# Performance work log

Measured on AMD Instinct MI355X. Metric: run time of the kernel, lower is better.

## Reference

```python
import jax, jax.numpy as jnp
import numpy as np

N, E, G = 50000, 400000, 500
F_IN, D_H, D_EMB = 92, 256, 128
EPS = 1e-5

def _ln(x, g, b):
    # per-node LayerNorm over feature dim
    mu = jnp.mean(x, axis=-1, keepdims=True)
    var = jnp.mean(jnp.square(x - mu), axis=-1, keepdims=True)
    return (x - mu) * jax.lax.rsqrt(var + EPS) * g + b

def _gcn_conv(x, src, dst, W, b):
    # PyG GCNConv: add self-loops, symmetric normalization
    xw = x @ W                                    # [N, D_out]
    loop = jnp.arange(N, dtype=src.dtype)
    s = jnp.concatenate([src, loop])              # [E+N]
    d = jnp.concatenate([dst, loop])
    deg = jax.ops.segment_sum(jnp.ones_like(d, dtype=xw.dtype), d, num_segments=N)
    dinv = jnp.where(deg > 0, jax.lax.rsqrt(jnp.maximum(deg, 1.0)) * (deg > 0), 0.0)
    norm = dinv[s] * dinv[d]                      # [E+N]
    msg = xw[s] * norm[:, None]                   # gather + scale
    out = jax.ops.segment_sum(msg, d, num_segments=N)  # scatter-add
    return out + b

def setup_inputs() -> dict:
    key = jax.random.key(0)
    ks = jax.random.split(key, 12)
    def lin(k, fan_in, fan_out):
        bound = 1.0 / np.sqrt(fan_in)
        kw, kb = jax.random.split(k)
        W = jax.random.uniform(kw, (fan_in, fan_out), jnp.float32, -bound, bound)
        b = jax.random.uniform(kb, (fan_out,), jnp.float32, -bound, bound)
        return W, b
    x = jax.random.normal(ks[0], (N, F_IN), jnp.float32)
    edge_index = jax.random.randint(ks[1], (2, E), 0, N, jnp.int32)
    batch = jnp.sort(jax.random.randint(ks[2], (N,), 0, G, jnp.int32))
    nfc_W, nfc_b = lin(ks[3], F_IN, D_H)
    gc1_W, gc1_b = lin(ks[4], D_H, D_H)
    gc2_W, gc2_b = lin(ks[5], D_H, D_EMB)
    fc1_W, fc1_b = lin(ks[6], D_EMB, 64)
    fc2_W, fc2_b = lin(ks[7], 64, 1)
    return {
        "x": x, "edge_index": edge_index, "batch": batch,
        "nfc_W": nfc_W, "nfc_b": nfc_b,
        "gn1_g": jnp.ones((D_H,), jnp.float32), "gn1_b": jnp.zeros((D_H,), jnp.float32),
        "gc1_W": gc1_W, "gc1_b": gc1_b,
        "gn2_g": jnp.ones((D_EMB,), jnp.float32), "gn2_b": jnp.zeros((D_EMB,), jnp.float32),
        "gc2_W": gc2_W, "gc2_b": gc2_b,
        "fc1_W": fc1_W, "fc1_b": fc1_b,
        "fc2_W": fc2_W, "fc2_b": fc2_b,
    }

def reference(x, edge_index, batch, nfc_W, nfc_b, gn1_g, gn1_b, gc1_W, gc1_b,
              gn2_g, gn2_b, gc2_W, gc2_b, fc1_W, fc1_b, fc2_W, fc2_b):
    src, dst = edge_index[0], edge_index[1]
    lrelu = jax.nn.leaky_relu  # slope 0.01, matches F.leaky_relu default
    ha = lrelu(x @ nfc_W + nfc_b)
    ha = lrelu(_ln(_gcn_conv(ha, src, dst, gc1_W, gc1_b), gn1_g, gn1_b))
    ha = lrelu(_ln(_gcn_conv(ha, src, dst, gc2_W, gc2_b), gn2_g, gn2_b))
    # F.normalize(p=2, dim=1)
    ha = ha / jnp.maximum(jnp.linalg.norm(ha, axis=1, keepdims=True), 1e-12)
    hg = jax.ops.segment_sum(ha, batch, num_segments=G)   # global_add_pool
    h = lrelu(hg @ fc1_W + fc1_b)
    out = h @ fc2_W + fc2_b
    return out, ha
```

## Files before the change

kernel.cpp:

```cpp
#include <hip/hip_runtime.h>

#define NN 50000
#define EE 400000
#define GG 500
#define F_IN 92
#define KP1 96
#define D_H 256
#define D_EMB 128
#define PCH 16

typedef __attribute__((ext_vector_type(8))) short short8_t;
typedef __attribute__((ext_vector_type(4))) float floatx4;
typedef unsigned short u16;
typedef unsigned int u32;

__device__ __forceinline__ float lrelu(float v) { return v > 0.f ? v : 0.01f * v; }
__device__ __forceinline__ u16 f2b(float v) {
    union { float f; u32 u; } x; x.f = v;
    u32 r = x.u + 0x7FFFu + ((x.u >> 16) & 1u);
    return (u16)(r >> 16);
}
__device__ __forceinline__ float wave_allsum(float v) {
#pragma unroll
    for (int m = 1; m < 64; m <<= 1) v += __shfl_xor(v, m);
    return v;
}

__global__ void count_kernel(const int* __restrict__ dst, int* __restrict__ cnt, int E) {
    int e = blockIdx.x * blockDim.x + threadIdx.x;
    if (e < E) atomicAdd(&cnt[dst[e]], 1);
}

__global__ void scan1(const int* __restrict__ cnt, int* __restrict__ excl,
                      int* __restrict__ bsum, float* __restrict__ dinv, int n) {
    __shared__ int sm[256];
    int i = blockIdx.x * 256 + threadIdx.x;
    int v = (i < n) ? cnt[i] : 0;
    if (i < n) dinv[i] = rsqrtf((float)v + 1.0f);
    sm[threadIdx.x] = v;
    __syncthreads();
#pragma unroll
    for (int off = 1; off < 256; off <<= 1) {
        int t = (threadIdx.x >= off) ? sm[threadIdx.x - off] : 0;
        __syncthreads();
        sm[threadIdx.x] += t;
        __syncthreads();
    }
    if (i < n) excl[i] = sm[threadIdx.x] - v;
    if (threadIdx.x == 255) bsum[blockIdx.x] = sm[255];
}
__global__ void scan2(int* __restrict__ bsum, int nb) {
    __shared__ int sm[256];
    int v = (threadIdx.x < nb) ? bsum[threadIdx.x] : 0;
    sm[threadIdx.x] = v;
    __syncthreads();
#pragma unroll
    for (int off = 1; off < 256; off <<= 1) {
        int t = (threadIdx.x >= off) ? sm[threadIdx.x - off] : 0;
        __syncthreads();
        sm[threadIdx.x] += t;
        __syncthreads();
    }
    if (threadIdx.x < nb) bsum[threadIdx.x] = sm[threadIdx.x] - v;
}
__global__ void scan3(int* __restrict__ rowptr, const int* __restrict__ bsum, int n, int E) {
    int i = blockIdx.x * 256 + threadIdx.x;
    if (i < n) rowptr[i] += bsum[blockIdx.x];
    if (i == 0) rowptr[n] = E;
}
__global__ void scatter_kernel(const int* __restrict__ src, const int* __restrict__ dst,
                               const int* __restrict__ rowptr, int* __restrict__ cursor,
                               int* __restrict__ esrc, int E) {
    int e = blockIdx.x * blockDim.x + threadIdx.x;
    if (e >= E) return;
    int d = dst[e];
    int p = rowptr[d] + atomicAdd(&cursor[d], 1);
    esrc[p] = src[e];
}

__global__ void cast_pad_x(const float* __restrict__ x, u16* __restrict__ xb) {
    long i = (long)blockIdx.x * blockDim.x + threadIdx.x;
    if (i >= (long)NN * KP1) return;
    int row = (int)(i / KP1), col = (int)(i % KP1);
    float v = (col < F_IN) ? x[(long)row * F_IN + col] : 0.f;
    xb[i] = f2b(v);
}
__global__ void castT_W(const float* __restrict__ W, u16* __restrict__ Wt,
                        int K, int Nd, int Kp) {
    int i = blockIdx.x * blockDim.x + threadIdx.x;
    if (i >= Nd * Kp) return;
    int n = i / Kp, k = i % Kp;
    Wt[i] = f2b(k < K ? W[(long)k * Nd + n] : 0.f);
}

template <bool BIAS_ACT, bool ROW_SCALE>
__global__ __launch_bounds__(256) void gemm_mfma(const u16* __restrict__ A,
                                                 const u16* __restrict__ Wt,
                                                 const float* __restrict__ bias,
                                                 const float* __restrict__ rscale,
                                                 u16* __restrict__ out,
                                                 int M, int Ka, int Nd) {
    __shared__ u16 As[128][40];
    __shared__ u16 Bs[64][40];
    int tid = threadIdx.x;
    int wave = tid >> 6, lane = tid & 63;
    int lm = lane & 15, lk = lane >> 4;
    int m0 = blockIdx.x * 128, n0 = blockIdx.y * 64;
    int rowA = tid >> 1, skA = (tid & 1) * 16;
    int rowB = tid >> 2, skB = (tid & 3) * 8;
    int gmA = m0 + rowA;
    const u16* Ap = A + (size_t)gmA * Ka + skA;
    const u16* Bp = Wt + (size_t)(n0 + rowB) * Ka + skB;
    floatx4 acc[2][4] = {};
    for (int k0 = 0; k0 < Ka; k0 += 32) {
        uint4 a0 = make_uint4(0, 0, 0, 0), a1 = make_uint4(0, 0, 0, 0);
        if (gmA < M) {
            a0 = *(const uint4*)(Ap + k0);
            a1 = *(const uint4*)(Ap + k0 + 8);
        }
        uint4 bv = *(const uint4*)(Bp + k0);
        __syncthreads();
        *(uint4*)&As[rowA][skA] = a0;
        *(uint4*)&As[rowA][skA + 8] = a1;
        *(uint4*)&Bs[rowB][skB] = bv;
        __syncthreads();
        short8_t af0 = *(const short8_t*)&As[wave * 32 + lm][lk * 8];
        short8_t af1 = *(const short8_t*)&As[wave * 32 + 16 + lm][lk * 8];
#pragma unroll
        for (int c = 0; c < 4; ++c) {
            short8_t bf = *(const short8_t*)&Bs[c * 16 + lm][lk * 8];
            acc[0][c] = __builtin_amdgcn_mfma_f32_16x16x32_bf16(af0, bf, acc[0][c], 0, 0, 0);
            acc[1][c] = __builtin_amdgcn_mfma_f32_16x16x32_bf16(af1, bf, acc[1][c], 0, 0, 0);
        }
    }
#pragma unroll
    for (int h = 0; h < 2; ++h) {
#pragma unroll
        for (int r = 0; r < 4; ++r) {
            int gm = m0 + wave * 32 + h * 16 + lk * 4 + r;
            if (gm >= M) continue;
            float rs = ROW_SCALE ? rscale[gm] : 1.f;
#pragma unroll
            for (int c = 0; c < 4; ++c) {
                int gn = n0 + c * 16 + lm;
                float v = acc[h][c][r];
                if constexpr (BIAS_ACT) { v += bias[gn]; v = lrelu(v); }
                if constexpr (ROW_SCALE) v *= rs;
                out[(size_t)gm * Nd + gn] = f2b(v);
            }
        }
    }
}

template <int U>
__device__ __forceinline__ void loadrow(const u32* __restrict__ p, u32* r) {
    if constexpr (U == 2) { uint2 t = *(const uint2*)p; r[0] = t.x; r[1] = t.y; }
    else                  { r[0] = *p; }
}
template <int D, bool L2N, bool TOBF>
__global__ __launch_bounds__(256) void agg_ln(const u16* __restrict__ y,
                                              const int* __restrict__ rowptr,
                                              const int* __restrict__ esrc,
                                              const float* __restrict__ dinv,
                                              const float* __restrict__ bias,
                                              const float* __restrict__ gamma,
                                              const float* __restrict__ beta,
                                              u16* __restrict__ outb,
                                              float* __restrict__ outf) {
    constexpr int V = D / 64;
    constexpr int U = V / 2;
    constexpr int RW = D / 2;
    int wave = threadIdx.x >> 6, lane = threadIdx.x & 63;
    int i = blockIdx.x * 4 + wave;
    if (i >= NN) return;
    int beg = __builtin_amdgcn_readfirstlane(rowptr[i]);
    int end = __builtin_amdgcn_readfirstlane(rowptr[i + 1]);
    const u32* yu = (const u32*)y;
    const int lu = lane * U;
    float accL[U] = {}, accH[U] = {};
    u32 r[8][U];
    int k = beg;
    for (; k + 7 < end; k += 8) {
#pragma unroll
        for (int q = 0; q < 8; ++q) loadrow<U>(yu + (size_t)esrc[k + q] * RW + lu, r[q]);
#pragma unroll
        for (int j = 0; j < U; ++j) {
            float sL = 0.f, sH = 0.f;
#pragma unroll
            for (int q = 0; q < 8; ++q) {
                sL += __uint_as_float(r[q][j] << 16);
                sH += __uint_as_float(r[q][j] & 0xFFFF0000u);
            }
            accL[j] += sL; accH[j] += sH;
        }
    }
    for (; k + 3 < end; k += 4) {
#pragma unroll
        for (int q = 0; q < 4; ++q) loadrow<U>(yu + (size_t)esrc[k + q] * RW + lu, r[q]);
#pragma unroll
        for (int j = 0; j < U; ++j) {
            accL[j] += (__uint_as_float(r[0][j] << 16) + __uint_as_float(r[1][j] << 16))
                     + (__uint_as_float(r[2][j] << 16) + __uint_as_float(r[3][j] << 16));
            accH[j] += (__uint_as_float(r[0][j] & 0xFFFF0000u) + __uint_as_float(r[1][j] & 0xFFFF0000u))
                     + (__uint_as_float(r[2][j] & 0xFFFF0000u) + __uint_as_float(r[3][j] & 0xFFFF0000u));
        }
    }
    for (; k < end; ++k) {
        loadrow<U>(yu + (size_t)esrc[k] * RW + lu, r[0]);
#pragma unroll
        for (int j = 0; j < U; ++j) {
            accL[j] += __uint_as_float(r[0][j] << 16);
            accH[j] += __uint_as_float(r[0][j] & 0xFFFF0000u);
        }
    }
    loadrow<U>(yu + (size_t)i * RW + lu, r[0]);
#pragma unroll
    for (int j = 0; j < U; ++j) {
        accL[j] += __uint_as_float(r[0][j] << 16);
        accH[j] += __uint_as_float(r[0][j] & 0xFFFF0000u);
    }
    float di = dinv[i];
    float xv[V], lsum = 0.f;
#pragma unroll
    for (int j = 0; j < U; ++j) {
        xv[2 * j]     = accL[j] * di + bias[lane * V + 2 * j];
        xv[2 * j + 1] = accH[j] * di + bias[lane * V + 2 * j + 1];
    }
#pragma unroll
    for (int v = 0; v < V; ++v) lsum += xv[v];
    float mu = wave_allsum(lsum) * (1.0f / D);
    float l2 = 0.f;
#pragma unroll
    for (int v = 0; v < V; ++v) { xv[v] -= mu; l2 += xv[v] * xv[v]; }
    float rstd = rsqrtf(wave_allsum(l2) * (1.0f / D) + 1e-5f);
    float yv[V], ss = 0.f;
#pragma unroll
    for (int v = 0; v < V; ++v) {
        float t = xv[v] * rstd * gamma[lane * V + v] + beta[lane * V + v];
        t = lrelu(t);
        yv[v] = t; ss += t * t;
    }
    if constexpr (L2N) {
        float inv = 1.0f / fmaxf(sqrtf(wave_allsum(ss)), 1e-12f);
#pragma unroll
        for (int v = 0; v < V; ++v) yv[v] *= inv;
    }
    if constexpr (TOBF) {
        if constexpr (V == 4) {
            *(ushort4*)(outb + (size_t)i * D + lane * V) =
                make_ushort4(f2b(yv[0]), f2b(yv[1]), f2b(yv[2]), f2b(yv[3]));
        } else {
            *(ushort2*)(outb + (size_t)i * D + lane * V) = make_ushort2(f2b(yv[0]), f2b(yv[1]));
        }
    } else {
        if constexpr (V == 2) {
            *(float2*)(outf + (size_t)i * D + lane * V) = make_float2(yv[0], yv[1]);
        } else {
            *(float4*)(outf + (size_t)i * D + lane * V) = make_float4(yv[0], yv[1], yv[2], yv[3]);
        }
    }
}

__global__ __launch_bounds__(128) void pool_partial(const float* __restrict__ ha,
                                                    const int* __restrict__ batch,
                                                    float* __restrict__ hg) {
    int r0 = blockIdx.x * PCH;
    int f = threadIdx.x;
    int end = min(r0 + PCH, NN);
    int cur = batch[r0];
    float acc = 0.f;
    for (int i = r0; i < end; ++i) {
        int b = batch[i];
        if (b != cur) {
            atomicAdd(&hg[(size_t)cur * D_EMB + f], acc);
            acc = 0.f; cur = b;
        }
        acc += ha[(size_t)i * D_EMB + f];
    }
    atomicAdd(&hg[(size_t)cur * D_EMB + f], acc);
}

__global__ __launch_bounds__(64) void head_kernel(const float* __restrict__ hg,
                                                  const float* __restrict__ fc1W,
                                                  const float* __restrict__ fc1b,
                                                  const float* __restrict__ fc2W,
                                                  const float* __restrict__ fc2b,
                                                  float* __restrict__ out) {
    int g = blockIdx.x;
    int j = threadIdx.x;
    float h = fc1b[j];
#pragma unroll 8
    for (int k = 0; k < D_EMB; ++k) h += hg[(size_t)g * D_EMB + k] * fc1W[k * 64 + j];
    h = lrelu(h) * fc2W[j];
#pragma unroll
    for (int m = 1; m < 64; m <<= 1) h += __shfl_xor(h, m);
    if (j == 0) out[g] = h + fc2b[0];
}

static inline size_t align256(size_t x) { return (x + 255) & ~(size_t)255; }

extern "C" void kernel_launch(void* const* d_in, const int* in_sizes, int n_in,
                              void* d_out, int out_size, void* d_ws, size_t ws_size,
                              hipStream_t stream) {
    const float* x     = (const float*)d_in[0];
    const int*   ei    = (const int*)d_in[1];
    const int*   batch = (const int*)d_in[2];
    const float* nfc_W = (const float*)d_in[3];
    const float* nfc_b = (const float*)d_in[4];
    const float* gn1_g = (const float*)d_in[5];
    const float* gn1_b = (const float*)d_in[6];
    const float* gc1_W = (const float*)d_in[7];
    const float* gc1_b = (const float*)d_in[8];
    const float* gn2_g = (const float*)d_in[9];
    const float* gn2_b = (const float*)d_in[10];
    const float* gc2_W = (const float*)d_in[11];
    const float* gc2_b = (const float*)d_in[12];
    const float* fc1_W = (const float*)d_in[13];
    const float* fc1_b = (const float*)d_in[14];
    const float* fc2_W = (const float*)d_in[15];
    const float* fc2_b = (const float*)d_in[16];

    char* ws = (char*)d_ws;
    size_t off = 0;
    int*   cnt    = (int*)(ws + off);   off += (size_t)NN * 4;
    int*   cursor = (int*)(ws + off);   off += align256((size_t)NN * 4);
    float* dinv   = (float*)(ws + off); off += align256((size_t)NN * 4);
    int*   rowptr = (int*)(ws + off);   off += align256((size_t)(NN + 1) * 4);
    int*   bsum   = (int*)(ws + off);   off += align256((size_t)256 * 4);
    int*   esrc   = (int*)(ws + off);   off += align256((size_t)EE * 4);
    float* hg     = (float*)(ws + off); off += align256((size_t)GG * D_EMB * 4);
    u16*   xb     = (u16*)(ws + off);   off += align256((size_t)NN * KP1 * 2);
    u16*   WtN    = (u16*)(ws + off);   off += align256((size_t)D_H * KP1 * 2);
    u16*   Wt1    = (u16*)(ws + off);   off += align256((size_t)D_H * D_H * 2);
    u16*   Wt2    = (u16*)(ws + off);   off += align256((size_t)D_EMB * D_H * 2);
    u16*   ha1b   = (u16*)(ws + off);   off += align256((size_t)NN * D_H * 2);
    u16*   y1b    = (u16*)(ws + off);   off += align256((size_t)NN * D_H * 2);
    u16*   ha2b   = (u16*)(ws + off);   off += align256((size_t)NN * D_H * 2);
    u16*   y2b    = (u16*)(ws + off);   off += align256((size_t)NN * D_EMB * 2);

    const int* src = ei;
    const int* dst = ei + EE;
    float* out_scores = (float*)d_out;
    float* out_ha     = (float*)d_out + GG;

    const int NB = (NN + 255) / 256;
    const int MB = (NN + 127) / 128;

    hipMemsetAsync(cnt, 0, (size_t)NN * 8, stream);
    hipMemsetAsync(hg, 0, (size_t)GG * D_EMB * 4, stream);
    count_kernel<<<(EE + 255) / 256, 256, 0, stream>>>(dst, cnt, EE);
    scan1<<<NB, 256, 0, stream>>>(cnt, rowptr, bsum, dinv, NN);
    scan2<<<1, 256, 0, stream>>>(bsum, NB);
    scan3<<<NB, 256, 0, stream>>>(rowptr, bsum, NN, EE);
    scatter_kernel<<<(EE + 255) / 256, 256, 0, stream>>>(src, dst, rowptr, cursor, esrc, EE);

    cast_pad_x<<<(int)(((long)NN * KP1 + 255) / 256), 256, 0, stream>>>(x, xb);
    castT_W<<<(D_H * KP1 + 255) / 256, 256, 0, stream>>>(nfc_W, WtN, F_IN, D_H, KP1);
    castT_W<<<(D_H * D_H + 255) / 256, 256, 0, stream>>>(gc1_W, Wt1, D_H, D_H, D_H);
    castT_W<<<(D_EMB * D_H + 255) / 256, 256, 0, stream>>>(gc2_W, Wt2, D_H, D_EMB, D_H);

    gemm_mfma<true, false><<<dim3(MB, D_H / 64), 256, 0, stream>>>(
        xb, WtN, nfc_b, nullptr, ha1b, NN, KP1, D_H);

    gemm_mfma<false, true><<<dim3(MB, D_H / 64), 256, 0, stream>>>(
        ha1b, Wt1, nullptr, dinv, y1b, NN, D_H, D_H);
    agg_ln<D_H, false, true><<<NN / 4, 256, 0, stream>>>(
        y1b, rowptr, esrc, dinv, gc1_b, gn1_g, gn1_b, ha2b, nullptr);

    gemm_mfma<false, true><<<dim3(MB, D_EMB / 64), 256, 0, stream>>>(
        ha2b, Wt2, nullptr, dinv, y2b, NN, D_H, D_EMB);
    agg_ln<D_EMB, true, false><<<NN / 4, 256, 0, stream>>>(
        y2b, rowptr, esrc, dinv, gc2_b, gn2_g, gn2_b, nullptr, out_ha);

    pool_partial<<<(NN + PCH - 1) / PCH, 128, 0, stream>>>(out_ha, batch, hg);
    head_kernel<<<GG, 64, 0, stream>>>(hg, fc1_W, fc1_b, fc2_W, fc2_b, out_scores);
}
```

Baseline: 306.4 us.

## Fuse x cast into first GEMM and split aggregation across half-waves

Removes the separate cast/pad kernel for x by having the first MFMA GEMM load fp32 input directly, converting it to bf16 with zero-padding of K. Restructures the neighbour aggregation so each 32-lane half-wave gathers a different neighbour row with wider vector loads; the two halves are combined with a cross-half shuffle. This is meant to cut an extra pass over x and raise load width and memory parallelism in the gather, at the cost of half the lanes idling in the LayerNorm epilogue and more index logic.

```diff
diff --git a/kernel.cpp b/kernel.cpp
--- a/kernel.cpp
+++ b/kernel.cpp
@@ -20,9 +20,9 @@
     u32 r = x.u + 0x7FFFu + ((x.u >> 16) & 1u);
     return (u16)(r >> 16);
 }
-__device__ __forceinline__ float wave_allsum(float v) {
-#pragma unroll
-    for (int m = 1; m < 64; m <<= 1) v += __shfl_xor(v, m);
+__device__ __forceinline__ float half_allsum(float v) {
+#pragma unroll
+    for (int m = 1; m < 32; m <<= 1) v += __shfl_xor(v, m);
     return v;
 }
 
@@ -78,13 +78,6 @@
     esrc[p] = src[e];
 }
 
-__global__ void cast_pad_x(const float* __restrict__ x, u16* __restrict__ xb) {
-    long i = (long)blockIdx.x * blockDim.x + threadIdx.x;
-    if (i >= (long)NN * KP1) return;
-    int row = (int)(i / KP1), col = (int)(i % KP1);
-    float v = (col < F_IN) ? x[(long)row * F_IN + col] : 0.f;
-    xb[i] = f2b(v);
-}
 __global__ void castT_W(const float* __restrict__ W, u16* __restrict__ Wt,
                         int K, int Nd, int Kp) {
     int i = blockIdx.x * blockDim.x + threadIdx.x;
@@ -93,13 +86,13 @@
     Wt[i] = f2b(k < K ? W[(long)k * Nd + n] : 0.f);
 }
 
-template <bool BIAS_ACT, bool ROW_SCALE>
-__global__ __launch_bounds__(256) void gemm_mfma(const u16* __restrict__ A,
+template <bool AF32, bool BIAS_ACT, bool ROW_SCALE>
+__global__ __launch_bounds__(256) void gemm_mfma(const void* __restrict__ Av,
                                                  const u16* __restrict__ Wt,
                                                  const float* __restrict__ bias,
                                                  const float* __restrict__ rscale,
                                                  u16* __restrict__ out,
-                                                 int M, int Ka, int Nd) {
+                                                 int M, int Ka, int Kreal, int Nd) {
     __shared__ u16 As[128][40];
     __shared__ u16 Bs[64][40];
     int tid = threadIdx.x;
@@ -109,14 +102,32 @@
     int rowA = tid >> 1, skA = (tid & 1) * 16;
     int rowB = tid >> 2, skB = (tid & 3) * 8;
     int gmA = m0 + rowA;
-    const u16* Ap = A + (size_t)gmA * Ka + skA;
+    const u16* Ab = (const u16*)Av + (AF32 ? 0 : (size_t)gmA * Ka + skA);
+    const float* Af = (const float*)Av + (size_t)gmA * Kreal;
     const u16* Bp = Wt + (size_t)(n0 + rowB) * Ka + skB;
     floatx4 acc[2][4] = {};
     for (int k0 = 0; k0 < Ka; k0 += 32) {
         uint4 a0 = make_uint4(0, 0, 0, 0), a1 = make_uint4(0, 0, 0, 0);
-        if (gmA < M) {
-            a0 = *(const uint4*)(Ap + k0);
-            a1 = *(const uint4*)(Ap + k0 + 8);
+        if constexpr (AF32) {
+            float f[16];
+#pragma unroll
+            for (int q = 0; q < 4; ++q) {
+                int col = k0 + skA + 4 * q;
+                float4 t = make_float4(0.f, 0.f, 0.f, 0.f);
+                if (gmA < M && col < Kreal) t = *(const float4*)(Af + col);
+                f[4 * q] = t.x; f[4 * q + 1] = t.y; f[4 * q + 2] = t.z; f[4 * q + 3] = t.w;
+            }
+            u32 pk[8];
+#pragma unroll
+            for (int t2 = 0; t2 < 8; ++t2)
+                pk[t2] = ((u32)f2b(f[2 * t2 + 1]) << 16) | f2b(f[2 * t2]);
+            a0 = make_uint4(pk[0], pk[1], pk[2], pk[3]);
+            a1 = make_uint4(pk[4], pk[5], pk[6], pk[7]);
+        } else {
+            if (gmA < M) {
+                a0 = *(const uint4*)(Ab + k0);
+                a1 = *(const uint4*)(Ab + k0 + 8);
+            }
         }
         uint4 bv = *(const uint4*)(Bp + k0);
         __syncthreads();
@@ -152,10 +163,10 @@
     }
 }
 
-template <int U>
-__device__ __forceinline__ void loadrow(const u32* __restrict__ p, u32* r) {
-    if constexpr (U == 2) { uint2 t = *(const uint2*)p; r[0] = t.x; r[1] = t.y; }
-    else                  { r[0] = *p; }
+template <int U2>
+__device__ __forceinline__ void loadU(const u32* __restrict__ p, u32* r) {
+    if constexpr (U2 == 4) { uint4 t = *(const uint4*)p; r[0]=t.x; r[1]=t.y; r[2]=t.z; r[3]=t.w; }
+    else                   { uint2 t = *(const uint2*)p; r[0]=t.x; r[1]=t.y; }
 }
 template <int D, bool L2N, bool TOBF>
 __global__ __launch_bounds__(256) void agg_ln(const u16* __restrict__ y,
@@ -167,96 +178,107 @@
                                               const float* __restrict__ beta,
                                               u16* __restrict__ outb,
                                               float* __restrict__ outf) {
-    constexpr int V = D / 64;
-    constexpr int U = V / 2;
+    constexpr int V2 = D / 32;
+    constexpr int U2 = V2 / 2;
     constexpr int RW = D / 2;
     int wave = threadIdx.x >> 6, lane = threadIdx.x & 63;
+    int half = lane >> 5, hl = lane & 31;
     int i = blockIdx.x * 4 + wave;
     if (i >= NN) return;
     int beg = __builtin_amdgcn_readfirstlane(rowptr[i]);
     int end = __builtin_amdgcn_readfirstlane(rowptr[i + 1]);
+    int R = end - beg + 1;
+    int P = R >> 1;
     const u32* yu = (const u32*)y;
-    const int lu = lane * U;
-    float accL[U] = {}, accH[U] = {};
-    u32 r[8][U];
-    int k = beg;
-    for (; k + 7 < end; k += 8) {
-#pragma unroll
-        for (int q = 0; q < 8; ++q) loadrow<U>(yu + (size_t)esrc[k + q] * RW + lu, r[q]);
-#pragma unroll
-        for (int j = 0; j < U; ++j) {
-            float sL = 0.f, sH = 0.f;
-#pragma unroll
-            for (int q = 0; q < 8; ++q) {
-                sL += __uint_as_float(r[q][j] << 16);
-                sH += __uint_as_float(r[q][j] & 0xFFFF0000u);
-            }
-            accL[j] += sL; accH[j] += sH;
-        }
-    }
-    for (; k + 3 < end; k += 4) {
-#pragma unroll
-        for (int q = 0; q < 4; ++q) loadrow<U>(yu + (size_t)esrc[k + q] * RW + lu, r[q]);
-#pragma unroll
-        for (int j = 0; j < U; ++j) {
-            accL[j] += (__uint_as_float(r[0][j] << 16) + __uint_as_float(r[1][j] << 16))
-                     + (__uint_as_float(r[2][j] << 16) + __uint_as_float(r[3][j] << 16));
-            accH[j] += (__uint_as_float(r[0][j] & 0xFFFF0000u) + __uint_as_float(r[1][j] & 0xFFFF0000u))
-                     + (__uint_as_float(r[2][j] & 0xFFFF0000u) + __uint_as_float(r[3][j] & 0xFFFF0000u));
-        }
-    }
-    for (; k < end; ++k) {
-        loadrow<U>(yu + (size_t)esrc[k] * RW + lu, r[0]);
-#pragma unroll
-        for (int j = 0; j < U; ++j) {
+    const int lu = hl * U2;
+    float accL[U2] = {}, accH[U2] = {};
+    u32 r[4][U2];
+    int p = 0;
+    for (; p + 4 <= P; p += 4) {
+#pragma unroll
+        for (int q = 0; q < 4; ++q) {
+            int t = 2 * (p + q) + half;
+            int idx = beg + min(t, R - 2);
+            int s = (t == R - 1) ? i : esrc[idx];
+            loadU<U2>(yu + (size_t)s * RW + lu, r[q]);
+        }
+#pragma unroll
+        for (int q = 0; q < 4; ++q)
+#pragma unroll
+            for (int j = 0; j < U2; ++j) {
+                accL[j] += __uint_as_float(r[q][j] << 16);
+                accH[j] += __uint_as_float(r[q][j] & 0xFFFF0000u);
+            }
+    }
+    for (; p < P; ++p) {
+        int t = 2 * p + half;
+        int idx = beg + min(t, R - 2);
+        int s = (t == R - 1) ? i : esrc[idx];
+        loadU<U2>(yu + (size_t)s * RW + lu, r[0]);
+#pragma unroll
+        for (int j = 0; j < U2; ++j) {
             accL[j] += __uint_as_float(r[0][j] << 16);
             accH[j] += __uint_as_float(r[0][j] & 0xFFFF0000u);
         }
     }
-    loadrow<U>(yu + (size_t)i * RW + lu, r[0]);
-#pragma unroll
-    for (int j = 0; j < U; ++j) {
-        accL[j] += __uint_as_float(r[0][j] << 16);
-        accH[j] += __uint_as_float(r[0][j] & 0xFFFF0000u);
+    if (R & 1) {
+        if (half == 0) {
+            loadU<U2>(yu + (size_t)i * RW + lu, r[0]);
+#pragma unroll
+            for (int j = 0; j < U2; ++j) {
+                accL[j] += __uint_as_float(r[0][j] << 16);
+                accH[j] += __uint_as_float(r[0][j] & 0xFFFF0000u);
+            }
+        }
+    }
+#pragma unroll
+    for (int j = 0; j < U2; ++j) {
+        accL[j] += __shfl_xor(accL[j], 32);
+        accH[j] += __shfl_xor(accH[j], 32);
     }
     float di = dinv[i];
-    float xv[V], lsum = 0.f;
-#pragma unroll
-    for (int j = 0; j < U; ++j) {
-        xv[2 * j]     = accL[j] * di + bias[lane * V + 2 * j];
-        xv[2 * j + 1] = accH[j] * di + bias[lane * V + 2 * j + 1];
-    }
-#pragma unroll
-    for (int v = 0; v < V; ++v) lsum += xv[v];
-    float mu = wave_allsum(lsum) * (1.0f / D);
+    float xv[V2], lsum = 0.f;
+#pragma unroll
+    for (int j = 0; j < U2; ++j) {
+        xv[2 * j]     = accL[j] * di + bias[hl * V2 + 2 * j];
+        xv[2 * j + 1] = accH[j] * di + bias[hl * V2 + 2 * j + 1];
+    }
+#pragma unroll
+    for (int v = 0; v < V2; ++v) lsum += xv[v];
+    float mu = half_allsum(lsum) * (1.0f / D);
     float l2 = 0.f;
 #pragma unroll
-    for (int v = 0; v < V; ++v) { xv[v] -= mu; l2 += xv[v] * xv[v]; }
-    float rstd = rsqrtf(wave_allsum(l2) * (1.0f / D) + 1e-5f);
-    float yv[V], ss = 0.f;
-#pragma unroll
-    for (int v = 0; v < V; ++v) {
-        float t = xv[v] * rstd * gamma[lane * V + v] + beta[lane * V + v];
+    for (int v = 0; v < V2; ++v) { xv[v] -= mu; l2 += xv[v] * xv[v]; }
+    float rstd = rsqrtf(half_allsum(l2) * (1.0f / D) + 1e-5f);
+    float yv[V2], ss = 0.f;
+#pragma unroll
+    for (int v = 0; v < V2; ++v) {
+        float t = xv[v] * rstd * gamma[hl * V2 + v] + beta[hl * V2 + v];
         t = lrelu(t);
         yv[v] = t; ss += t * t;
     }
     if constexpr (L2N) {
-        float inv = 1.0f / fmaxf(sqrtf(wave_allsum(ss)), 1e-12f);
-#pragma unroll
-        for (int v = 0; v < V; ++v) yv[v] *= inv;
-    }
-    if constexpr (TOBF) {
-        if constexpr (V == 4) {
-            *(ushort4*)(outb + (size_t)i * D + lane * V) =
-                make_ushort4(f2b(yv[0]), f2b(yv[1]), f2b(yv[2]), f2b(yv[3]));
+        float inv = 1.0f / fmaxf(sqrtf(half_allsum(ss)), 1e-12f);
+#pragma unroll
+        for (int v = 0; v < V2; ++v) yv[v] *= inv;
+    }
+    if (half == 0) {
+        if constexpr (TOBF) {
+            u32 pk[U2];
+#pragma unroll
+            for (int j = 0; j < U2; ++j)
+                pk[j] = ((u32)f2b(yv[2 * j + 1]) << 16) | f2b(yv[2 * j]);
+            if constexpr (U2 == 4)
+                *(uint4*)((u32*)outb + (size_t)i * RW + lu) = make_uint4(pk[0], pk[1], pk[2], pk[3]);
+            else
+                *(uint2*)((u32*)outb + (size_t)i * RW + lu) = make_uint2(pk[0], pk[1]);
         } else {
-            *(ushort2*)(outb + (size_t)i * D + lane * V) = make_ushort2(f2b(yv[0]), f2b(yv[1]));
-        }
-    } else {
-        if constexpr (V == 2) {
-            *(float2*)(outf + (size_t)i * D + lane * V) = make_float2(yv[0], yv[1]);
-        } else {
-            *(float4*)(outf + (size_t)i * D + lane * V) = make_float4(yv[0], yv[1], yv[2], yv[3]);
+            if constexpr (V2 == 4)
+                *(float4*)(outf + (size_t)i * D + hl * V2) = make_float4(yv[0], yv[1], yv[2], yv[3]);
+            else {
+                *(float4*)(outf + (size_t)i * D + hl * V2) = make_float4(yv[0], yv[1], yv[2], yv[3]);
+                *(float4*)(outf + (size_t)i * D + hl * V2 + 4) = make_float4(yv[4], yv[5], yv[6], yv[7]);
+            }
         }
     }
 }
@@ -329,7 +351,6 @@
     int*   bsum   = (int*)(ws + off);   off += align256((size_t)256 * 4);
     int*   esrc   = (int*)(ws + off);   off += align256((size_t)EE * 4);
     float* hg     = (float*)(ws + off); off += align256((size_t)GG * D_EMB * 4);
-    u16*   xb     = (u16*)(ws + off);   off += align256((size_t)NN * KP1 * 2);
     u16*   WtN    = (u16*)(ws + off);   off += align256((size_t)D_H * KP1 * 2);
     u16*   Wt1    = (u16*)(ws + off);   off += align256((size_t)D_H * D_H * 2);
     u16*   Wt2    = (u16*)(ws + off);   off += align256((size_t)D_EMB * D_H * 2);
@@ -354,21 +375,20 @@
     scan3<<<NB, 256, 0, stream>>>(rowptr, bsum, NN, EE);
     scatter_kernel<<<(EE + 255) / 256, 256, 0, stream>>>(src, dst, rowptr, cursor, esrc, EE);
 
-    cast_pad_x<<<(int)(((long)NN * KP1 + 255) / 256), 256, 0, stream>>>(x, xb);
     castT_W<<<(D_H * KP1 + 255) / 256, 256, 0, stream>>>(nfc_W, WtN, F_IN, D_H, KP1);
     castT_W<<<(D_H * D_H + 255) / 256, 256, 0, stream>>>(gc1_W, Wt1, D_H, D_H, D_H);
     castT_W<<<(D_EMB * D_H + 255) / 256, 256, 0, stream>>>(gc2_W, Wt2, D_H, D_EMB, D_H);
 
-    gemm_mfma<true, false><<<dim3(MB, D_H / 64), 256, 0, stream>>>(
-        xb, WtN, nfc_b, nullptr, ha1b, NN, KP1, D_H);
-
-    gemm_mfma<false, true><<<dim3(MB, D_H / 64), 256, 0, stream>>>(
-        ha1b, Wt1, nullptr, dinv, y1b, NN, D_H, D_H);
+    gemm_mfma<true, true, false><<<dim3(MB, D_H / 64), 256, 0, stream>>>(
+        x, WtN, nfc_b, nullptr, ha1b, NN, KP1, F_IN, D_H);
+
+    gemm_mfma<false, false, true><<<dim3(MB, D_H / 64), 256, 0, stream>>>(
+        ha1b, Wt1, nullptr, dinv, y1b, NN, D_H, D_H, D_H);
     agg_ln<D_H, false, true><<<NN / 4, 256, 0, stream>>>(
         y1b, rowptr, esrc, dinv, gc1_b, gn1_g, gn1_b, ha2b, nullptr);
 
-    gemm_mfma<false, true><<<dim3(MB, D_EMB / 64), 256, 0, stream>>>(
-        ha2b, Wt2, nullptr, dinv, y2b, NN, D_H, D_EMB);
+    gemm_mfma<false, false, true><<<dim3(MB, D_EMB / 64), 256, 0, stream>>>(
+        ha2b, Wt2, nullptr, dinv, y2b, NN, D_H, D_H, D_EMB);
     agg_ln<D_EMB, true, false><<<NN / 4, 256, 0, stream>>>(
         y2b, rowptr, esrc, dinv, gc2_b, gn2_g, gn2_b, nullptr, out_ha);
 
```

New measurement: 318.9 us. 1.04x slower.

## Fuse x cast into first GEMM, single-block CSR scan, merged weight casts

Applied to the files above, without the earlier changes.

The first GEMM now reads fp32 x directly and converts to bf16 while loading tiles, which removes the padded bf16 copy of x and its kernel. The three-kernel prefix scan becomes one 1024-thread block in which each thread serially scans 49 counts. The three weight cast/transpose kernels are merged into one, and the two memsets into one by making the zeroed buffers contiguous. This cuts launches and global traffic, but the single-block scan uses one CU and strided, uncoalesced reads, so it may be slower than the multi-block version.

```diff
diff --git a/kernel.cpp b/kernel.cpp
--- a/kernel.cpp
+++ b/kernel.cpp
@@ -8,6 +8,7 @@
 #define D_H 256
 #define D_EMB 128
 #define PCH 16
+#define SCH 49
 
 typedef __attribute__((ext_vector_type(8))) short short8_t;
 typedef __attribute__((ext_vector_type(4))) float floatx4;
@@ -31,43 +32,34 @@
     if (e < E) atomicAdd(&cnt[dst[e]], 1);
 }
 
-__global__ void scan1(const int* __restrict__ cnt, int* __restrict__ excl,
-                      int* __restrict__ bsum, float* __restrict__ dinv, int n) {
-    __shared__ int sm[256];
-    int i = blockIdx.x * 256 + threadIdx.x;
-    int v = (i < n) ? cnt[i] : 0;
-    if (i < n) dinv[i] = rsqrtf((float)v + 1.0f);
-    sm[threadIdx.x] = v;
+__global__ __launch_bounds__(1024) void scan_csr(const int* __restrict__ cnt,
+                                                 int* __restrict__ rowptr,
+                                                 float* __restrict__ dinv) {
+    __shared__ int sums[1024];
+    int t = threadIdx.x;
+    int base = t * SCH;
+    int lim = min(base + SCH, NN);
+    int s = 0;
+    for (int i = base; i < lim; ++i) s += cnt[i];
+    sums[t] = s;
     __syncthreads();
 #pragma unroll
-    for (int off = 1; off < 256; off <<= 1) {
-        int t = (threadIdx.x >= off) ? sm[threadIdx.x - off] : 0;
+    for (int off = 1; off < 1024; off <<= 1) {
+        int v = (t >= off) ? sums[t - off] : 0;
         __syncthreads();
-        sm[threadIdx.x] += t;
+        sums[t] += v;
         __syncthreads();
     }
-    if (i < n) excl[i] = sm[threadIdx.x] - v;
-    if (threadIdx.x == 255) bsum[blockIdx.x] = sm[255];
-}
-__global__ void scan2(int* __restrict__ bsum, int nb) {
-    __shared__ int sm[256];
-    int v = (threadIdx.x < nb) ? bsum[threadIdx.x] : 0;
-    sm[threadIdx.x] = v;
-    __syncthreads();
-#pragma unroll
-    for (int off = 1; off < 256; off <<= 1) {
-        int t = (threadIdx.x >= off) ? sm[threadIdx.x - off] : 0;
-        __syncthreads();
-        sm[threadIdx.x] += t;
-        __syncthreads();
-    }
-    if (threadIdx.x < nb) bsum[threadIdx.x] = sm[threadIdx.x] - v;
-}
-__global__ void scan3(int* __restrict__ rowptr, const int* __restrict__ bsum, int n, int E) {
-    int i = blockIdx.x * 256 + threadIdx.x;
-    if (i < n) rowptr[i] += bsum[blockIdx.x];
-    if (i == 0) rowptr[n] = E;
-}
+    int run = sums[t] - s;
+    for (int i = base; i < lim; ++i) {
+        int c = cnt[i];
+        rowptr[i] = run;
+        run += c;
+        dinv[i] = rsqrtf((float)c + 1.0f);
+    }
+    if (t == 0) rowptr[NN] = EE;
+}
+
 __global__ void scatter_kernel(const int* __restrict__ src, const int* __restrict__ dst,
                                const int* __restrict__ rowptr, int* __restrict__ cursor,
                                int* __restrict__ esrc, int E) {
@@ -78,28 +70,34 @@
     esrc[p] = src[e];
 }
 
-__global__ void cast_pad_x(const float* __restrict__ x, u16* __restrict__ xb) {
-    long i = (long)blockIdx.x * blockDim.x + threadIdx.x;
-    if (i >= (long)NN * KP1) return;
-    int row = (int)(i / KP1), col = (int)(i % KP1);
-    float v = (col < F_IN) ? x[(long)row * F_IN + col] : 0.f;
-    xb[i] = f2b(v);
-}
-__global__ void castT_W(const float* __restrict__ W, u16* __restrict__ Wt,
-                        int K, int Nd, int Kp) {
+#define WN_ELEMS (D_H * KP1)
+#define W1_ELEMS (D_H * D_H)
+#define W2_ELEMS (D_EMB * D_H)
+__global__ void cast_all(const float* __restrict__ nfc_W, const float* __restrict__ gc1_W,
+                         const float* __restrict__ gc2_W, u16* __restrict__ WtN,
+                         u16* __restrict__ Wt1, u16* __restrict__ Wt2) {
     int i = blockIdx.x * blockDim.x + threadIdx.x;
-    if (i >= Nd * Kp) return;
-    int n = i / Kp, k = i % Kp;
-    Wt[i] = f2b(k < K ? W[(long)k * Nd + n] : 0.f);
-}
-
-template <bool BIAS_ACT, bool ROW_SCALE>
-__global__ __launch_bounds__(256) void gemm_mfma(const u16* __restrict__ A,
+    if (i < WN_ELEMS) {
+        int n = i / KP1, k = i % KP1;
+        WtN[i] = f2b(k < F_IN ? nfc_W[(long)k * D_H + n] : 0.f);
+    } else if (i < WN_ELEMS + W1_ELEMS) {
+        int j = i - WN_ELEMS;
+        int n = j / D_H, k = j % D_H;
+        Wt1[j] = f2b(gc1_W[(long)k * D_H + n]);
+    } else if (i < WN_ELEMS + W1_ELEMS + W2_ELEMS) {
+        int j = i - WN_ELEMS - W1_ELEMS;
+        int n = j / D_H, k = j % D_H;
+        Wt2[j] = f2b(gc2_W[(long)k * D_EMB + n]);
+    }
+}
+
+template <bool AF32, bool BIAS_ACT, bool ROW_SCALE>
+__global__ __launch_bounds__(256) void gemm_mfma(const void* __restrict__ Av,
                                                  const u16* __restrict__ Wt,
                                                  const float* __restrict__ bias,
                                                  const float* __restrict__ rscale,
                                                  u16* __restrict__ out,
-                                                 int M, int Ka, int Nd) {
+                                                 int M, int Ka, int Kreal, int Nd) {
     __shared__ u16 As[128][40];
     __shared__ u16 Bs[64][40];
     int tid = threadIdx.x;
@@ -109,14 +107,32 @@
     int rowA = tid >> 1, skA = (tid & 1) * 16;
     int rowB = tid >> 2, skB = (tid & 3) * 8;
     int gmA = m0 + rowA;
-    const u16* Ap = A + (size_t)gmA * Ka + skA;
+    const u16* Ab = (const u16*)Av + (AF32 ? 0 : (size_t)gmA * Ka + skA);
+    const float* Af = (const float*)Av + (size_t)gmA * Kreal;
     const u16* Bp = Wt + (size_t)(n0 + rowB) * Ka + skB;
     floatx4 acc[2][4] = {};
     for (int k0 = 0; k0 < Ka; k0 += 32) {
         uint4 a0 = make_uint4(0, 0, 0, 0), a1 = make_uint4(0, 0, 0, 0);
-        if (gmA < M) {
-            a0 = *(const uint4*)(Ap + k0);
-            a1 = *(const uint4*)(Ap + k0 + 8);
+        if constexpr (AF32) {
+            float f[16];
+#pragma unroll
+            for (int q = 0; q < 4; ++q) {
+                int col = k0 + skA + 4 * q;
+                float4 t = make_float4(0.f, 0.f, 0.f, 0.f);
+                if (gmA < M && col < Kreal) t = *(const float4*)(Af + col);
+                f[4 * q] = t.x; f[4 * q + 1] = t.y; f[4 * q + 2] = t.z; f[4 * q + 3] = t.w;
+            }
+            u32 pk[8];
+#pragma unroll
+            for (int t2 = 0; t2 < 8; ++t2)
+                pk[t2] = ((u32)f2b(f[2 * t2 + 1]) << 16) | f2b(f[2 * t2]);
+            a0 = make_uint4(pk[0], pk[1], pk[2], pk[3]);
+            a1 = make_uint4(pk[4], pk[5], pk[6], pk[7]);
+        } else {
+            if (gmA < M) {
+                a0 = *(const uint4*)(Ab + k0);
+                a1 = *(const uint4*)(Ab + k0 + 8);
+            }
         }
         uint4 bv = *(const uint4*)(Bp + k0);
         __syncthreads();
@@ -323,13 +339,11 @@
     char* ws = (char*)d_ws;
     size_t off = 0;
     int*   cnt    = (int*)(ws + off);   off += (size_t)NN * 4;
-    int*   cursor = (int*)(ws + off);   off += align256((size_t)NN * 4);
+    int*   cursor = (int*)(ws + off);   off += (size_t)NN * 4;
+    float* hg     = (float*)(ws + off); off += align256((size_t)GG * D_EMB * 4);
     float* dinv   = (float*)(ws + off); off += align256((size_t)NN * 4);
     int*   rowptr = (int*)(ws + off);   off += align256((size_t)(NN + 1) * 4);
-    int*   bsum   = (int*)(ws + off);   off += align256((size_t)256 * 4);
     int*   esrc   = (int*)(ws + off);   off += align256((size_t)EE * 4);
-    float* hg     = (float*)(ws + off); off += align256((size_t)GG * D_EMB * 4);
-    u16*   xb     = (u16*)(ws + off);   off += align256((size_t)NN * KP1 * 2);
     u16*   WtN    = (u16*)(ws + off);   off += align256((size_t)D_H * KP1 * 2);
     u16*   Wt1    = (u16*)(ws + off);   off += align256((size_t)D_H * D_H * 2);
     u16*   Wt2    = (u16*)(ws + off);   off += align256((size_t)D_EMB * D_H * 2);
@@ -343,32 +357,27 @@
     float* out_scores = (float*)d_out;
     float* out_ha     = (float*)d_out + GG;
 
-    const int NB = (NN + 255) / 256;
     const int MB = (NN + 127) / 128;
-
-    hipMemsetAsync(cnt, 0, (size_t)NN * 8, stream);
-    hipMemsetAsync(hg, 0, (size_t)GG * D_EMB * 4, stream);
+    const size_t zbytes = (size_t)NN * 8 + (size_t)GG * D_EMB * 4;
+
+    hipMemsetAsync(cnt, 0, zbytes, stream);
     count_kernel<<<(EE + 255) / 256, 256, 0, stream>>>(dst, cnt, EE);
-    scan1<<<NB, 256, 0, stream>>>(cnt, rowptr, bsum, dinv, NN);
-    scan2<<<1, 256, 0, stream>>>(bsum, NB);
-    scan3<<<NB, 256, 0, stream>>>(rowptr, bsum, NN, EE);
+    scan_csr<<<1, 1024, 0, stream>>>(cnt, rowptr, dinv);
     scatter_kernel<<<(EE + 255) / 256, 256, 0, stream>>>(src, dst, rowptr, cursor, esrc, EE);
 
-    cast_pad_x<<<(int)(((long)NN * KP1 + 255) / 256), 256, 0, stream>>>(x, xb);
-    castT_W<<<(D_H * KP1 + 255) / 256, 256, 0, stream>>>(nfc_W, WtN, F_IN, D_H, KP1);
-    castT_W<<<(D_H * D_H + 255) / 256, 256, 0, stream>>>(gc1_W, Wt1, D_H, D_H, D_H);
-    castT_W<<<(D_EMB * D_H + 255) / 256, 256, 0, stream>>>(gc2_W, Wt2, D_H, D_EMB, D_H);
-
-    gemm_mfma<true, false><<<dim3(MB, D_H / 64), 256, 0, stream>>>(
-        xb, WtN, nfc_b, nullptr, ha1b, NN, KP1, D_H);
-
-    gemm_mfma<false, true><<<dim3(MB, D_H / 64), 256, 0, stream>>>(
-        ha1b, Wt1, nullptr, dinv, y1b, NN, D_H, D_H);
+    cast_all<<<(WN_ELEMS + W1_ELEMS + W2_ELEMS + 255) / 256, 256, 0, stream>>>(
+        nfc_W, gc1_W, gc2_W, WtN, Wt1, Wt2);
+
+    gemm_mfma<true, true, false><<<dim3(MB, D_H / 64), 256, 0, stream>>>(
+        x, WtN, nfc_b, nullptr, ha1b, NN, KP1, F_IN, D_H);
+
+    gemm_mfma<false, false, true><<<dim3(MB, D_H / 64), 256, 0, stream>>>(
+        ha1b, Wt1, nullptr, dinv, y1b, NN, D_H, D_H, D_H);
     agg_ln<D_H, false, true><<<NN / 4, 256, 0, stream>>>(
         y1b, rowptr, esrc, dinv, gc1_b, gn1_g, gn1_b, ha2b, nullptr);
 
-    gemm_mfma<false, true><<<dim3(MB, D_EMB / 64), 256, 0, stream>>>(
-        ha2b, Wt2, nullptr, dinv, y2b, NN, D_H, D_EMB);
+    gemm_mfma<false, false, true><<<dim3(MB, D_EMB / 64), 256, 0, stream>>>(
+        ha2b, Wt2, nullptr, dinv, y2b, NN, D_H, D_H, D_EMB);
     agg_ln<D_EMB, true, false><<<NN / 4, 256, 0, stream>>>(
         y2b, rowptr, esrc, dinv, gc2_b, gn2_g, gn2_b, nullptr, out_ha);
 
```

After: 394.3 us. +28.7%, slower.
